# Kernel optimization log

Measured on AMD Instinct MI355X. Metric: run time of the kernel, lower is better.

The kernel has to match this reference:

```python
import jax, jax.numpy as jnp
import numpy as np

N_NODES = 50000
N_EDGES = 600000
DIM = 128
K = 3
N_LAYERS = 3
LEAKY_SLOPE = 0.01  # nn.LeakyReLU default
RE_NORM = 1.0       # 2/lambda_max with lambda_max=2 (standard ChebNet approximation)


def setup_inputs() -> dict:
    key = jax.random.key(0)
    ks = jax.random.split(key, 8)
    weights = jax.random.normal(ks[0], (N_NODES,), dtype=jnp.float32)
    src = jax.random.randint(ks[1], (N_EDGES,), 0, N_NODES)
    dst = jax.random.randint(ks[2], (N_EDGES,), 0, N_NODES)
    lin_in_w = jax.random.normal(ks[3], (1, DIM), dtype=jnp.float32) * 0.5
    lin_in_b = jnp.zeros((DIM,), dtype=jnp.float32)
    cheb_ws = jax.random.normal(ks[4], (N_LAYERS, K * DIM, DIM), dtype=jnp.float32) * 0.05
    cheb_bs = jnp.zeros((N_LAYERS, DIM), dtype=jnp.float32)
    pred_w = jax.random.normal(ks[5], (DIM, 1), dtype=jnp.float32) * 0.05
    pred_b = jnp.zeros((1,), dtype=jnp.float32)
    return {"weights": weights, "src": src, "dst": dst,
            "lin_in_w": lin_in_w, "lin_in_b": lin_in_b,
            "cheb_ws": cheb_ws, "cheb_bs": cheb_bs,
            "pred_w": pred_w, "pred_b": pred_b}


def _cheb_conv(x, W, b, src, dst, d_invsqrt, n):
    # DGL ChebConv with lambda_max=2 -> re_norm=1: scaled Laplacian L_hat = -D^-1/2 A D^-1/2
    def spmm(f):  # unnormalized Laplacian-style aggregation: D^-1/2 A D^-1/2 f
        h = f * d_invsqrt
        agg = jax.ops.segment_sum(h[src], dst, num_segments=n)
        return agg * d_invsqrt

    X0 = x
    terms = [X0]
    h = spmm(X0)
    X1 = -RE_NORM * h + X0 * (RE_NORM - 1.0)
    terms.append(X1)
    for _ in range(2, K):
        h = spmm(X1)
        Xi = -2.0 * RE_NORM * h + X1 * (2.0 * (RE_NORM - 1.0)) - X0
        terms.append(Xi)
        X0, X1 = X1, Xi
    Xt = jnp.concatenate(terms, axis=1)  # [N, K*DIM]
    return jax.nn.relu(Xt @ W + b)       # DGL ChebConv default activation=F.relu


def reference(weights, src, dst, lin_in_w, lin_in_b, cheb_ws, cheb_bs, pred_w, pred_b):
    n = weights.shape[0]
    # dgl.add_self_loop
    loop = jnp.arange(n, dtype=src.dtype)
    src_f = jnp.concatenate([src, loop])
    dst_f = jnp.concatenate([dst, loop])
    # in-degree normalization D^-1/2 (clamp min 1)
    deg = jax.ops.segment_sum(jnp.ones_like(dst_f, dtype=jnp.float32), dst_f, num_segments=n)
    d_invsqrt = jnp.power(jnp.clip(deg, 1.0), -0.5)[:, None]  # [N,1]

    feat = weights[:, None] @ lin_in_w + lin_in_b             # [N, DIM]
    emb = _cheb_conv(feat, cheb_ws[0], cheb_bs[0], src_f, dst_f, d_invsqrt, n)
    for i in range(1, N_LAYERS):
        emb = jax.nn.leaky_relu(emb, negative_slope=LEAKY_SLOPE)
        emb = _cheb_conv(emb, cheb_ws[i], cheb_bs[i], src_f, dst_f, d_invsqrt, n)
    logits = emb @ pred_w + pred_b                            # do_train=True path
    return logits
```

## Files before the change

### kernel.cpp

```cpp
#include <hip/hip_runtime.h>

typedef unsigned int uint;
typedef unsigned short ushort;

#define NN 50000
#define NE 600000
#define DIM 128
#define KD 384
#define PADK 40

typedef __attribute__((ext_vector_type(8))) short short8;
typedef __attribute__((ext_vector_type(4))) float float4v;

static __device__ __forceinline__ ushort f2b(float f) {
    uint u = __float_as_uint(f);
    return (ushort)((u + 0x7FFFu + ((u >> 16) & 1u)) >> 16);
}
static __device__ __forceinline__ float blo(uint u) { return __uint_as_float(u << 16); }
static __device__ __forceinline__ float bhi(uint u) { return __uint_as_float(u & 0xFFFF0000u); }
static __device__ __forceinline__ float asf(uint u) { return __uint_as_float(u); }

__global__ void k_init(int* __restrict__ cnt, const float* __restrict__ cw,
                       ushort* __restrict__ wt, const float* __restrict__ lw,
                       const float* __restrict__ lb, float* __restrict__ uvout) {
    if (blockIdx.x < 49) {
        int i = blockIdx.x * 256 + threadIdx.x;
        if (i < 12544) ((int4*)cnt)[i] = make_int4(0, 0, 0, 0);
    } else if (blockIdx.x < 625) {
        int i = (blockIdx.x - 49) * 256 + threadIdx.x;
        if (i < 3 * KD * DIM) {
            int l = i / (KD * DIM), rem = i - l * (KD * DIM);
            int k = rem >> 7, n = rem & 127;
            wt[(size_t)l * KD * DIM + (size_t)n * KD + k] = f2b(cw[i]);
        }
    } else {
        int vec = blockIdx.x - 625;
        int t = vec >> 1;
        const float* coef = (vec & 1) ? lb : lw;
        int c = threadIdx.x;
        if (c < 128) {
            float s = 0.f;
#pragma unroll 8
            for (int k = 0; k < 128; ++k)
                s = fmaf(coef[k], cw[(size_t)(t * 128 + k) * 128 + c], s);
            uvout[vec * 128 + c] = s;
        }
    }
}

__global__ void k_hist(const int* __restrict__ dst, int* __restrict__ cnt,
                       int* __restrict__ rank) {
    int e = blockIdx.x * 256 + threadIdx.x;
    if (e < NE) rank[e] = atomicAdd(&cnt[dst[e]], 1);
}

__global__ __launch_bounds__(256) void k_scan1(const int* __restrict__ cnt,
                                               int* __restrict__ incl,
                                               int* __restrict__ bsums,
                                               const float* __restrict__ w,
                                               uint2* __restrict__ nrec) {
    __shared__ int sh[256];
    int i = blockIdx.x * 256 + threadIdx.x;
    int v = (i < NN) ? cnt[i] : 0;
    if (i < NN) {
        uint2 r;
        r.x = __float_as_uint(rsqrtf((float)(v + 1)));
        r.y = __float_as_uint(w[i]);
        nrec[i] = r;
    }
    sh[threadIdx.x] = v;
    __syncthreads();
    for (int d = 1; d < 256; d <<= 1) {
        int t = (threadIdx.x >= d) ? sh[threadIdx.x - d] : 0;
        __syncthreads();
        sh[threadIdx.x] += t;
        __syncthreads();
    }
    incl[i] = sh[threadIdx.x];
    if (threadIdx.x == 255) bsums[blockIdx.x] = sh[255];
}

__global__ __launch_bounds__(256) void k_scan3(const int* __restrict__ cnt,
                                               const int* __restrict__ incl,
                                               const int* __restrict__ bsums,
                                               int* __restrict__ offs) {
    __shared__ int sh[256];
    __shared__ int boff;
    int tid = threadIdx.x;
    int v = (tid < 196) ? bsums[tid] : 0;
    sh[tid] = v;
    __syncthreads();
    for (int d = 1; d < 256; d <<= 1) {
        int t = (tid >= d) ? sh[tid - d] : 0;
        __syncthreads();
        sh[tid] += t;
        __syncthreads();
    }
    if (tid == blockIdx.x) boff = sh[tid] - v;
    __syncthreads();
    int i = blockIdx.x * 256 + tid;
    if (i >= NN) return;
    offs[i] = incl[i] - cnt[i] + boff;
    if (i == NN - 1) offs[NN] = NE;
}

__global__ void k_fill4(const int* __restrict__ src, const int* __restrict__ dst,
                        const int* __restrict__ rank, const int* __restrict__ offs,
                        uint* __restrict__ csrS) {
    int e = blockIdx.x * 256 + threadIdx.x;
    if (e < NE) {
        int p = offs[dst[e]] + rank[e];
        csrS[p] = (uint)src[e];
    }
}

__global__ __launch_bounds__(256) void k_csrfin(
        const int* __restrict__ offs, const uint* __restrict__ csrS,
        const uint2* __restrict__ nrec, uint2* __restrict__ csrE,
        float2* __restrict__ SS) {
    int n = blockIdx.x * 16 + (threadIdx.x >> 4);
    int l = threadIdx.x & 15;
    int j0 = offs[n], j1 = offs[n + 1];
    uint2 nr_n = nrec[n];
    float dn = asf(nr_n.x);
    float sA = 0.f, sB = 0.f;
    for (int j = j0 + l; j < j1; j += 16) {
        uint s = csrS[j];
        uint2 nr = nrec[s];
        float ds = asf(nr.x);
        float wv = ds * dn;
        float hw = ds * asf(nr.y);
        uint2 rec;
        rec.x = s;
        rec.y = __float_as_uint(wv);
        csrE[j] = rec;
        sA += hw;
        sB += wv;
    }
#pragma unroll
    for (int off = 8; off > 0; off >>= 1) {
        sA += __shfl_down(sA, off, 16);
        sB += __shfl_down(sB, off, 16);
    }
    if (l == 0) {
        float id = dn * dn;
        float2 o;
        o.x = dn * sA + id * asf(nr_n.y);
        o.y = sB + id;
        SS[n] = o;
    }
}

__global__ __launch_bounds__(256) void k_spmv2l1(
        const int* __restrict__ offs, const uint2* __restrict__ csrE,
        const float2* __restrict__ SS, const uint2* __restrict__ nrec,
        const float* __restrict__ uv, const float* __restrict__ bias,
        ushort* __restrict__ Pb) {
    __shared__ float suv[768];
    __shared__ float sbias[128];
    int tid = threadIdx.x;
    for (int i = tid; i < 768; i += 256) suv[i] = uv[i];
    if (tid < 128) sbias[tid] = bias[tid];
    __syncthreads();

    int n = blockIdx.x * 16 + (tid >> 4);
    int l = tid & 15;
    int j0 = offs[n], j1 = offs[n + 1];
    float sC = 0.f, sD = 0.f;
    for (int j = j0 + l; j < j1; j += 16) {
        uint2 q = csrE[j];
        float wv = asf(q.y);
        float2 s = SS[q.x];
        sC = fmaf(wv, s.x, sC);
        sD = fmaf(wv, s.y, sD);
    }
#pragma unroll
    for (int off = 8; off > 0; off >>= 1) {
        sC += __shfl_down(sC, off, 16);
        sD += __shfl_down(sD, off, 16);
    }
    sC = __shfl(sC, 0, 16);
    sD = __shfl(sD, 0, 16);

    uint2 nr = nrec[n];
    float dn = asf(nr.x), id = dn * dn;
    float2 s = SS[n];
    float ssw = sC + id * s.x;
    float ss1 = sD + id * s.y;
    float a0 = asf(nr.y);
    float a1 = -s.x, b1 = -s.y;
    float a2 = 2.f * ssw - a0, b2 = 2.f * ss1 - 1.f;

    const float2* uv2 = (const float2*)suv;
    uint r[4];
#pragma unroll
    for (int q = 0; q < 4; ++q) {
        int p = 4 * l + q;
        float2 u0 = uv2[p],       v0 = uv2[64 + p];
        float2 u1 = uv2[128 + p], v1 = uv2[192 + p];
        float2 u2 = uv2[256 + p], v2 = uv2[320 + p];
        float2 bb = ((const float2*)sbias)[p];
        float o0 = bb.x + a0 * u0.x + v0.x + a1 * u1.x + b1 * v1.x + a2 * u2.x + b2 * v2.x;
        float o1 = bb.y + a0 * u0.y + v0.y + a1 * u1.y + b1 * v1.y + a2 * u2.y + b2 * v2.y;
        r[q] = (uint)f2b(fmaxf(o0, 0.f)) | ((uint)f2b(fmaxf(o1, 0.f)) << 16);
    }
    uint4 w4; w4.x = r[0]; w4.y = r[1]; w4.z = r[2]; w4.w = r[3];
    ((uint4*)(Pb + (size_t)n * DIM))[l] = w4;
}

__global__ __launch_bounds__(256) void k_gather1(
        const ushort* __restrict__ Xb, const int* __restrict__ offs,
        const uint2* __restrict__ csrE, const uint2* __restrict__ nrec,
        ushort* __restrict__ Qb) {
    int n = __builtin_amdgcn_readfirstlane(blockIdx.x * 4 + (threadIdx.x >> 6));
    int lane = threadIdx.x & 63;
    int j0 = offs[n], j1 = offs[n + 1];
    const uint* Xu = (const uint*)Xb;
    uint un = Xu[(size_t)n * 64 + lane];
    float dn = asf(nrec[n].x);
    float a0 = 0.f, a1 = 0.f;
#pragma unroll 8
    for (int j = j0; j < j1; ++j) {
        uint2 e = csrE[j];
        float wv = asf(e.y);
        uint u = Xu[(size_t)e.x * 64 + lane];
        a0 = fmaf(wv, blo(u), a0);
        a1 = fmaf(wv, bhi(u), a1);
    }
    float id = dn * dn;
    uint ow = (uint)f2b(-(a0 + blo(un) * id))
            | ((uint)f2b(-(a1 + bhi(un) * id)) << 16);
    ((uint*)Qb)[(size_t)n * 64 + lane] = ow;
}

__global__ __launch_bounds__(256) void k_gather2(
        const ushort* __restrict__ X1b, const ushort* __restrict__ X0b,
        const int* __restrict__ offs, const uint2* __restrict__ csrE,
        const uint2* __restrict__ nrec, ushort* __restrict__ Rb) {
    int n = __builtin_amdgcn_readfirstlane(blockIdx.x * 4 + (threadIdx.x >> 6));
    int lane = threadIdx.x & 63;
    int j0 = offs[n], j1 = offs[n + 1];
    const uint* Xu = (const uint*)X1b;
    uint u1n = Xu[(size_t)n * 64 + lane];
    uint u0n = ((const uint*)X0b)[(size_t)n * 64 + lane];
    float dn = asf(nrec[n].x);
    float a0 = 0.f, a1 = 0.f;
#pragma unroll 8
    for (int j = j0; j < j1; ++j) {
        uint2 e = csrE[j];
        float wv = asf(e.y);
        uint u = Xu[(size_t)e.x * 64 + lane];
        a0 = fmaf(wv, blo(u), a0);
        a1 = fmaf(wv, bhi(u), a1);
    }
    float id = dn * dn;
    uint ow = (uint)f2b(-2.f * (a0 + blo(u1n) * id) - blo(u0n))
            | ((uint)f2b(-2.f * (a1 + bhi(u1n) * id) - bhi(u0n)) << 16);
    ((uint*)Rb)[(size_t)n * 64 + lane] = ow;
}

__global__ __launch_bounds__(256) void k_gemm(
        const ushort* __restrict__ X0b, const ushort* __restrict__ X1b,
        const ushort* __restrict__ X2b, const ushort* __restrict__ Wt,
        const float* __restrict__ bias, ushort* __restrict__ outb) {
    __shared__ ushort As[128 * PADK];
    __shared__ ushort Bs[128 * PADK];
    int tid = threadIdx.x;
    int nbase = blockIdx.x * 128;
    int wave = tid >> 6, lane = tid & 63;
    int wr = wave >> 1, wc = wave & 1;
    int l15 = lane & 15, quad = lane >> 4;

    float4v acc[4][4];
#pragma unroll
    for (int i = 0; i < 4; ++i)
#pragma unroll
        for (int j = 0; j < 4; ++j) acc[i][j] = (float4v)0.f;

    int srow = tid >> 1, shalf = tid & 1;
    int gm = nbase + srow; if (gm >= NN) gm = NN - 1;

    for (int c = 0; c < 12; ++c) {
        int part = c >> 2;
        int k0 = (c & 3) * 32;
        const ushort* Xp = (part == 0) ? X0b : ((part == 1) ? X1b : X2b);
        const uint4* ga = (const uint4*)(Xp + (size_t)gm * DIM + k0 + shalf * 16);
        uint4 a0 = ga[0], a1 = ga[1];
        const uint4* gb = (const uint4*)(Wt + (size_t)srow * KD + c * 32 + shalf * 16);
        uint4 b0 = gb[0], b1 = gb[1];
        __syncthreads();
        uint4* pa = (uint4*)(As + srow * PADK + shalf * 16);
        pa[0] = a0; pa[1] = a1;
        uint4* pb = (uint4*)(Bs + srow * PADK + shalf * 16);
        pb[0] = b0; pb[1] = b1;
        __syncthreads();
        short8 af[4], bf[4];
#pragma unroll
        for (int i = 0; i < 4; ++i) {
            af[i] = *(const short8*)(As + (wr * 64 + i * 16 + l15) * PADK + quad * 8);
            bf[i] = *(const short8*)(Bs + (wc * 64 + i * 16 + l15) * PADK + quad * 8);
        }
#pragma unroll
        for (int i = 0; i < 4; ++i)
#pragma unroll
            for (int j = 0; j < 4; ++j)
                acc[i][j] = __builtin_amdgcn_mfma_f32_16x16x32_bf16(
                    af[i], bf[j], acc[i][j], 0, 0, 0);
    }

    float bv[4];
#pragma unroll
    for (int j = 0; j < 4; ++j) bv[j] = bias[wc * 64 + j * 16 + l15];
#pragma unroll
    for (int i = 0; i < 4; ++i) {
#pragma unroll
        for (int r = 0; r < 4; ++r) {
            int node = nbase + wr * 64 + i * 16 + quad * 4 + r;
            if (node < NN) {
#pragma unroll
                for (int j = 0; j < 4; ++j) {
                    int col = wc * 64 + j * 16 + l15;
                    outb[(size_t)node * DIM + col] =
                        f2b(fmaxf(acc[i][j][r] + bv[j], 0.f));
                }
            }
        }
    }
}

__global__ __launch_bounds__(256) void k_gemm_pred(
        const ushort* __restrict__ X0b, const ushort* __restrict__ X1b,
        const ushort* __restrict__ X2b, const ushort* __restrict__ Wt,
        const float* __restrict__ bias, const float* __restrict__ pw,
        const float* __restrict__ pb, float* __restrict__ logits) {
    __shared__ ushort As[128 * PADK];
    __shared__ ushort Bs[128 * PADK];
    __shared__ float lsum[128];
    int tid = threadIdx.x;
    int nbase = blockIdx.x * 128;
    int wave = tid >> 6, lane = tid & 63;
    int wr = wave >> 1, wc = wave & 1;
    int l15 = lane & 15, quad = lane >> 4;

    float4v acc[4][4];
#pragma unroll
    for (int i = 0; i < 4; ++i)
#pragma unroll
        for (int j = 0; j < 4; ++j) acc[i][j] = (float4v)0.f;

    int srow = tid >> 1, shalf = tid & 1;
    int gm = nbase + srow; if (gm >= NN) gm = NN - 1;

    for (int c = 0; c < 12; ++c) {
        int part = c >> 2;
        int k0 = (c & 3) * 32;
        const ushort* Xp = (part == 0) ? X0b : ((part == 1) ? X1b : X2b);
        const uint4* ga = (const uint4*)(Xp + (size_t)gm * DIM + k0 + shalf * 16);
        uint4 a0 = ga[0], a1 = ga[1];
        const uint4* gb = (const uint4*)(Wt + (size_t)srow * KD + c * 32 + shalf * 16);
        uint4 b0 = gb[0], b1 = gb[1];
        __syncthreads();
        uint4* pa = (uint4*)(As + srow * PADK + shalf * 16);
        pa[0] = a0; pa[1] = a1;
        uint4* pb2 = (uint4*)(Bs + srow * PADK + shalf * 16);
        pb2[0] = b0; pb2[1] = b1;
        __syncthreads();
        short8 af[4], bf[4];
#pragma unroll
        for (int i = 0; i < 4; ++i) {
            af[i] = *(const short8*)(As + (wr * 64 + i * 16 + l15) * PADK + quad * 8);
            bf[i] = *(const short8*)(Bs + (wc * 64 + i * 16 + l15) * PADK + quad * 8);
        }
#pragma unroll
        for (int i = 0; i < 4; ++i)
#pragma unroll
            for (int j = 0; j < 4; ++j)
                acc[i][j] = __builtin_amdgcn_mfma_f32_16x16x32_bf16(
                    af[i], bf[j], acc[i][j], 0, 0, 0);
    }

    __syncthreads();
    if (tid < 128) lsum[tid] = 0.f;
    __syncthreads();
    float bv[4], pwv[4];
#pragma unroll
    for (int j = 0; j < 4; ++j) {
        int col = wc * 64 + j * 16 + l15;
        bv[j] = bias[col];
        pwv[j] = pw[col];
    }
#pragma unroll
    for (int i = 0; i < 4; ++i) {
#pragma unroll
        for (int r = 0; r < 4; ++r) {
            float local = 0.f;
#pragma unroll
            for (int j = 0; j < 4; ++j)
                local = fmaf(fmaxf(acc[i][j][r] + bv[j], 0.f), pwv[j], local);
            local += __shfl_xor(local, 1, 64);
            local += __shfl_xor(local, 2, 64);
            local += __shfl_xor(local, 4, 64);
            local += __shfl_xor(local, 8, 64);
            if (l15 == 0)
                atomicAdd(&lsum[wr * 64 + i * 16 + quad * 4 + r], local);
        }
    }
    __syncthreads();
    if (tid < 128) {
        int node = nbase + tid;
        if (node < NN) logits[node] = lsum[tid] + pb[0];
    }
}

extern "C" void kernel_launch(void* const* d_in, const int* in_sizes, int n_in,
                              void* d_out, int out_size, void* d_ws, size_t ws_size,
                              hipStream_t stream) {
    int i_weights = 0, i_src = 1, i_dst = 2, i_lw = 3, i_lb = 4,
        i_cw = 5, i_cb = 6, i_pw = 7, i_pb = 8;
    {
        int seen600k = 0, seen128 = 0;
        for (int i = 0; i < n_in; ++i) {
            int s = in_sizes[i];
            if (s == 50000) i_weights = i;
            else if (s == 600000) { if (seen600k == 0) i_src = i; else i_dst = i; ++seen600k; }
            else if (s == 128) { if (seen128 == 0) i_lw = i; else if (seen128 == 1) i_lb = i; else i_pw = i; ++seen128; }
            else if (s == 147456) i_cw = i;
            else if (s == 384) i_cb = i;
            else if (s == 1) i_pb = i;
        }
    }
    const float* weights = (const float*)d_in[i_weights];
    const int*   src     = (const int*)d_in[i_src];
    const int*   dst     = (const int*)d_in[i_dst];
    const float* lin_w   = (const float*)d_in[i_lw];
    const float* lin_b   = (const float*)d_in[i_lb];
    const float* cheb_w  = (const float*)d_in[i_cw];
    const float* cheb_b  = (const float*)d_in[i_cb];
    const float* pred_w  = (const float*)d_in[i_pw];
    const float* pred_b  = (const float*)d_in[i_pb];
    float* out = (float*)d_out;

    uint2*  csrE    = (uint2*)d_ws;
    uint2*  nrec    = csrE + NE;
    float2* SS      = (float2*)(nrec + 50048);
    float*  uv      = (float*)(SS + 50048);
    int*    offs    = (int*)(uv + 768);
    int*    cnt     = offs + 50056;
    int*    incl    = cnt + 50176;
    int*    bsums   = incl + 50176;
    int*    rank    = bsums + 256;
    uint*   csrS    = (uint*)(rank + NE);
    ushort* Pb      = (ushort*)(csrS + NE);
    ushort* Qb      = Pb + (size_t)NN * DIM;
    ushort* Rb      = Qb + (size_t)NN * DIM;
    ushort* Wtb     = Rb + (size_t)NN * DIM;

    k_init<<<631, 256, 0, stream>>>(cnt, cheb_w, Wtb, lin_w, lin_b, uv);
    k_hist<<<2344, 256, 0, stream>>>(dst, cnt, rank);
    k_scan1<<<196, 256, 0, stream>>>(cnt, incl, bsums, weights, nrec);
    k_scan3<<<196, 256, 0, stream>>>(cnt, incl, bsums, offs);
    k_fill4<<<2344, 256, 0, stream>>>(src, dst, rank, offs, csrS);
    k_csrfin<<<3125, 256, 0, stream>>>(offs, csrS, nrec, csrE, SS);

    k_spmv2l1<<<3125, 256, 0, stream>>>(offs, csrE, SS, nrec, uv, cheb_b, Pb);

    k_gather1<<<12500, 256, 0, stream>>>(Pb, offs, csrE, nrec, Qb);
    k_gather2<<<12500, 256, 0, stream>>>(Qb, Pb, offs, csrE, nrec, Rb);
    k_gemm<<<391, 256, 0, stream>>>(Pb, Qb, Rb, Wtb + (size_t)KD * DIM,
                                    cheb_b + DIM, Pb);
    k_gather1<<<12500, 256, 0, stream>>>(Pb, offs, csrE, nrec, Qb);
    k_gather2<<<12500, 256, 0, stream>>>(Qb, Pb, offs, csrE, nrec, Rb);
    k_gemm_pred<<<391, 256, 0, stream>>>(Pb, Qb, Rb, Wtb + (size_t)2 * KD * DIM,
                                         cheb_b + 2 * DIM, pred_w, pred_b, out);
}
```

Before: 297.9 us.

## Fuse second Chebyshev gather into GEMM via shared-memory X2 tile

Removes the separate k_gather2 kernel. Each GEMM block now computes its own 128 rows of the third Chebyshev term into LDS, using 16 lanes per row with uint4 loads, and feeds them to the MFMA loop. This drops the global write and re-read of the X2 buffer and one launch per layer. In exchange the latency-bound sparse gather runs on only 391 blocks, with heavier LDS use per block, so occupancy and memory-level parallelism for the gather phase fall.

```diff
diff --git a/kernel.cpp b/kernel.cpp
--- a/kernel.cpp
+++ b/kernel.cpp
@@ -8,6 +8,7 @@
 #define DIM 128
 #define KD 384
 #define PADK 40
+#define X2P 136
 
 typedef __attribute__((ext_vector_type(8))) short short8;
 typedef __attribute__((ext_vector_type(4))) float float4v;
@@ -233,40 +234,60 @@
     ((uint*)Qb)[(size_t)n * 64 + lane] = ow;
 }
 
-__global__ __launch_bounds__(256) void k_gather2(
-        const ushort* __restrict__ X1b, const ushort* __restrict__ X0b,
+__global__ __launch_bounds__(256) void k_gemmf(
+        const ushort* __restrict__ X0b, const ushort* __restrict__ X1b,
         const int* __restrict__ offs, const uint2* __restrict__ csrE,
-        const uint2* __restrict__ nrec, ushort* __restrict__ Rb) {
-    int n = __builtin_amdgcn_readfirstlane(blockIdx.x * 4 + (threadIdx.x >> 6));
-    int lane = threadIdx.x & 63;
-    int j0 = offs[n], j1 = offs[n + 1];
-    const uint* Xu = (const uint*)X1b;
-    uint u1n = Xu[(size_t)n * 64 + lane];
-    uint u0n = ((const uint*)X0b)[(size_t)n * 64 + lane];
-    float dn = asf(nrec[n].x);
-    float a0 = 0.f, a1 = 0.f;
-#pragma unroll 8
-    for (int j = j0; j < j1; ++j) {
-        uint2 e = csrE[j];
-        float wv = asf(e.y);
-        uint u = Xu[(size_t)e.x * 64 + lane];
-        a0 = fmaf(wv, blo(u), a0);
-        a1 = fmaf(wv, bhi(u), a1);
-    }
-    float id = dn * dn;
-    uint ow = (uint)f2b(-2.f * (a0 + blo(u1n) * id) - blo(u0n))
-            | ((uint)f2b(-2.f * (a1 + bhi(u1n) * id) - bhi(u0n)) << 16);
-    ((uint*)Rb)[(size_t)n * 64 + lane] = ow;
-}
-
-__global__ __launch_bounds__(256) void k_gemm(
-        const ushort* __restrict__ X0b, const ushort* __restrict__ X1b,
-        const ushort* __restrict__ X2b, const ushort* __restrict__ Wt,
+        const uint2* __restrict__ nrec, const ushort* __restrict__ Wt,
         const float* __restrict__ bias, ushort* __restrict__ outb) {
     __shared__ ushort As[128 * PADK];
     __shared__ ushort Bs[128 * PADK];
+    __shared__ ushort X2s[128 * X2P];
     int tid = threadIdx.x;
     int nbase = blockIdx.x * 128;
+
+    {
+        int grp = tid >> 4;
+        int l = tid & 15;
+        const uint4* X1u4 = (const uint4*)X1b;
+        const uint4* X0u4 = (const uint4*)X0b;
+        for (int k = 0; k < 8; ++k) {
+            int row = grp * 8 + k;
+            int n = nbase + row;
+            uint4 w4;
+            if (n < NN) {
+                int j0 = offs[n], j1 = offs[n + 1];
+                float a0 = 0.f, a1 = 0.f, a2 = 0.f, a3 = 0.f;
+                float a4 = 0.f, a5 = 0.f, a6 = 0.f, a7 = 0.f;
+#pragma unroll 4
+                for (int j = j0; j < j1; ++j) {
+                    uint2 e = csrE[j];
+                    float wv = asf(e.y);
+                    uint4 u = X1u4[(size_t)e.x * 16 + l];
+                    a0 = fmaf(wv, blo(u.x), a0); a1 = fmaf(wv, bhi(u.x), a1);
+                    a2 = fmaf(wv, blo(u.y), a2); a3 = fmaf(wv, bhi(u.y), a3);
+                    a4 = fmaf(wv, blo(u.z), a4); a5 = fmaf(wv, bhi(u.z), a5);
+                    a6 = fmaf(wv, blo(u.w), a6); a7 = fmaf(wv, bhi(u.w), a7);
+                }
+                float dn = asf(nrec[n].x);
+                float id = dn * dn;
+                uint4 u1 = X1u4[(size_t)n * 16 + l];
+                uint4 u0 = X0u4[(size_t)n * 16 + l];
+                w4.x = (uint)f2b(-2.f * (a0 + blo(u1.x) * id) - blo(u0.x))
+                     | ((uint)f2b(-2.f * (a1 + bhi(u1.x) * id) - bhi(u0.x)) << 16);
+                w4.y = (uint)f2b(-2.f * (a2 + blo(u1.y) * id) - blo(u0.y))
+                     | ((uint)f2b(-2.f * (a3 + bhi(u1.y) * id) - bhi(u0.y)) << 16);
+                w4.z = (uint)f2b(-2.f * (a4 + blo(u1.z) * id) - blo(u0.z))
+                     | ((uint)f2b(-2.f * (a5 + bhi(u1.z) * id) - bhi(u0.z)) << 16);
+                w4.w = (uint)f2b(-2.f * (a6 + blo(u1.w) * id) - blo(u0.w))
+                     | ((uint)f2b(-2.f * (a7 + bhi(u1.w) * id) - bhi(u0.w)) << 16);
+            } else {
+                w4.x = 0; w4.y = 0; w4.z = 0; w4.w = 0;
+            }
+            *(uint4*)(X2s + (size_t)row * X2P + l * 8) = w4;
+        }
+    }
+    __syncthreads();
+
     int wave = tid >> 6, lane = tid & 63;
     int wr = wave >> 1, wc = wave & 1;
     int l15 = lane & 15, quad = lane >> 4;
@@ -283,21 +304,30 @@
     for (int c = 0; c < 12; ++c) {
         int part = c >> 2;
         int k0 = (c & 3) * 32;
-        const ushort* Xp = (part == 0) ? X0b : ((part == 1) ? X1b : X2b);
-        const uint4* ga = (const uint4*)(Xp + (size_t)gm * DIM + k0 + shalf * 16);
-        uint4 a0 = ga[0], a1 = ga[1];
+        uint4 a0, a1;
+        if (part < 2) {
+            const ushort* Xp = (part == 0) ? X0b : X1b;
+            const uint4* ga = (const uint4*)(Xp + (size_t)gm * DIM + k0 + shalf * 16);
+            a0 = ga[0]; a1 = ga[1];
+        }
         const uint4* gb = (const uint4*)(Wt + (size_t)srow * KD + c * 32 + shalf * 16);
         uint4 b0 = gb[0], b1 = gb[1];
         __syncthreads();
-        uint4* pa = (uint4*)(As + srow * PADK + shalf * 16);
-        pa[0] = a0; pa[1] = a1;
+        if (part < 2) {
+            uint4* pa = (uint4*)(As + srow * PADK + shalf * 16);
+            pa[0] = a0; pa[1] = a1;
+        }
         uint4* pb = (uint4*)(Bs + srow * PADK + shalf * 16);
         pb[0] = b0; pb[1] = b1;
         __syncthreads();
         short8 af[4], bf[4];
 #pragma unroll
         for (int i = 0; i < 4; ++i) {
-            af[i] = *(const short8*)(As + (wr * 64 + i * 16 + l15) * PADK + quad * 8);
+            if (part < 2)
+                af[i] = *(const short8*)(As + (wr * 64 + i * 16 + l15) * PADK + quad * 8);
+            else
+                af[i] = *(const short8*)(X2s + (size_t)(wr * 64 + i * 16 + l15) * X2P
+                                         + k0 + quad * 8);
             bf[i] = *(const short8*)(Bs + (wc * 64 + i * 16 + l15) * PADK + quad * 8);
         }
 #pragma unroll
@@ -328,16 +358,62 @@
     }
 }
 
-__global__ __launch_bounds__(256) void k_gemm_pred(
+__global__ __launch_bounds__(256) void k_gemmf_pred(
         const ushort* __restrict__ X0b, const ushort* __restrict__ X1b,
-        const ushort* __restrict__ X2b, const ushort* __restrict__ Wt,
+        const int* __restrict__ offs, const uint2* __restrict__ csrE,
+        const uint2* __restrict__ nrec, const ushort* __restrict__ Wt,
         const float* __restrict__ bias, const float* __restrict__ pw,
         const float* __restrict__ pb, float* __restrict__ logits) {
     __shared__ ushort As[128 * PADK];
     __shared__ ushort Bs[128 * PADK];
+    __shared__ ushort X2s[128 * X2P];
     __shared__ float lsum[128];
     int tid = threadIdx.x;
     int nbase = blockIdx.x * 128;
+
+    {
+        int grp = tid >> 4;
+        int l = tid & 15;
+        const uint4* X1u4 = (const uint4*)X1b;
+        const uint4* X0u4 = (const uint4*)X0b;
+        for (int k = 0; k < 8; ++k) {
+            int row = grp * 8 + k;
+            int n = nbase + row;
+            uint4 w4;
+            if (n < NN) {
+                int j0 = offs[n], j1 = offs[n + 1];
+                float a0 = 0.f, a1 = 0.f, a2 = 0.f, a3 = 0.f;
+                float a4 = 0.f, a5 = 0.f, a6 = 0.f, a7 = 0.f;
+#pragma unroll 4
+                for (int j = j0; j < j1; ++j) {
+                    uint2 e = csrE[j];
+                    float wv = asf(e.y);
+                    uint4 u = X1u4[(size_t)e.x * 16 + l];
+                    a0 = fmaf(wv, blo(u.x), a0); a1 = fmaf(wv, bhi(u.x), a1);
+                    a2 = fmaf(wv, blo(u.y), a2); a3 = fmaf(wv, bhi(u.y), a3);
+                    a4 = fmaf(wv, blo(u.z), a4); a5 = fmaf(wv, bhi(u.z), a5);
+                    a6 = fmaf(wv, blo(u.w), a6); a7 = fmaf(wv, bhi(u.w), a7);
+                }
+                float dn = asf(nrec[n].x);
+                float id = dn * dn;
+                uint4 u1 = X1u4[(size_t)n * 16 + l];
+                uint4 u0 = X0u4[(size_t)n * 16 + l];
+                w4.x = (uint)f2b(-2.f * (a0 + blo(u1.x) * id) - blo(u0.x))
+                     | ((uint)f2b(-2.f * (a1 + bhi(u1.x) * id) - bhi(u0.x)) << 16);
+                w4.y = (uint)f2b(-2.f * (a2 + blo(u1.y) * id) - blo(u0.y))
+                     | ((uint)f2b(-2.f * (a3 + bhi(u1.y) * id) - bhi(u0.y)) << 16);
+                w4.z = (uint)f2b(-2.f * (a4 + blo(u1.z) * id) - blo(u0.z))
+                     | ((uint)f2b(-2.f * (a5 + bhi(u1.z) * id) - bhi(u0.z)) << 16);
+                w4.w = (uint)f2b(-2.f * (a6 + blo(u1.w) * id) - blo(u0.w))
+                     | ((uint)f2b(-2.f * (a7 + bhi(u1.w) * id) - bhi(u0.w)) << 16);
+            } else {
+                w4.x = 0; w4.y = 0; w4.z = 0; w4.w = 0;
+            }
+            *(uint4*)(X2s + (size_t)row * X2P + l * 8) = w4;
+        }
+    }
+    __syncthreads();
+
     int wave = tid >> 6, lane = tid & 63;
     int wr = wave >> 1, wc = wave & 1;
     int l15 = lane & 15, quad = lane >> 4;
@@ -354,21 +430,30 @@
     for (int c = 0; c < 12; ++c) {
         int part = c >> 2;
         int k0 = (c & 3) * 32;
-        const ushort* Xp = (part == 0) ? X0b : ((part == 1) ? X1b : X2b);
-        const uint4* ga = (const uint4*)(Xp + (size_t)gm * DIM + k0 + shalf * 16);
-        uint4 a0 = ga[0], a1 = ga[1];
+        uint4 a0, a1;
+        if (part < 2) {
+            const ushort* Xp = (part == 0) ? X0b : X1b;
+            const uint4* ga = (const uint4*)(Xp + (size_t)gm * DIM + k0 + shalf * 16);
+            a0 = ga[0]; a1 = ga[1];
+        }
         const uint4* gb = (const uint4*)(Wt + (size_t)srow * KD + c * 32 + shalf * 16);
         uint4 b0 = gb[0], b1 = gb[1];
         __syncthreads();
-        uint4* pa = (uint4*)(As + srow * PADK + shalf * 16);
-        pa[0] = a0; pa[1] = a1;
+        if (part < 2) {
+            uint4* pa = (uint4*)(As + srow * PADK + shalf * 16);
+            pa[0] = a0; pa[1] = a1;
+        }
         uint4* pb2 = (uint4*)(Bs + srow * PADK + shalf * 16);
         pb2[0] = b0; pb2[1] = b1;
         __syncthreads();
         short8 af[4], bf[4];
 #pragma unroll
         for (int i = 0; i < 4; ++i) {
-            af[i] = *(const short8*)(As + (wr * 64 + i * 16 + l15) * PADK + quad * 8);
+            if (part < 2)
+                af[i] = *(const short8*)(As + (wr * 64 + i * 16 + l15) * PADK + quad * 8);
+            else
+                af[i] = *(const short8*)(X2s + (size_t)(wr * 64 + i * 16 + l15) * X2P
+                                         + k0 + quad * 8);
             bf[i] = *(const short8*)(Bs + (wc * 64 + i * 16 + l15) * PADK + quad * 8);
         }
 #pragma unroll
@@ -452,8 +537,7 @@
     uint*   csrS    = (uint*)(rank + NE);
     ushort* Pb      = (ushort*)(csrS + NE);
     ushort* Qb      = Pb + (size_t)NN * DIM;
-    ushort* Rb      = Qb + (size_t)NN * DIM;
-    ushort* Wtb     = Rb + (size_t)NN * DIM;
+    ushort* Wtb     = Qb + (size_t)NN * DIM;
 
     k_init<<<631, 256, 0, stream>>>(cnt, cheb_w, Wtb, lin_w, lin_b, uv);
     k_hist<<<2344, 256, 0, stream>>>(dst, cnt, rank);
@@ -465,11 +549,10 @@
     k_spmv2l1<<<3125, 256, 0, stream>>>(offs, csrE, SS, nrec, uv, cheb_b, Pb);
 
     k_gather1<<<12500, 256, 0, stream>>>(Pb, offs, csrE, nrec, Qb);
-    k_gather2<<<12500, 256, 0, stream>>>(Qb, Pb, offs, csrE, nrec, Rb);
-    k_gemm<<<391, 256, 0, stream>>>(Pb, Qb, Rb, Wtb + (size_t)KD * DIM,
-                                    cheb_b + DIM, Pb);
+    k_gemmf<<<391, 256, 0, stream>>>(Pb, Qb, offs, csrE, nrec,
+                                     Wtb + (size_t)KD * DIM, cheb_b + DIM, Pb);
     k_gather1<<<12500, 256, 0, stream>>>(Pb, offs, csrE, nrec, Qb);
-    k_gather2<<<12500, 256, 0, stream>>>(Qb, Pb, offs, csrE, nrec, Rb);
-    k_gemm_pred<<<391, 256, 0, stream>>>(Pb, Qb, Rb, Wtb + (size_t)2 * KD * DIM,
-                                         cheb_b + 2 * DIM, pred_w, pred_b, out);
-}
+    k_gemmf_pred<<<391, 256, 0, stream>>>(Pb, Qb, offs, csrE, nrec,
+                                          Wtb + (size_t)2 * KD * DIM,
+                                          cheb_b + 2 * DIM, pred_w, pred_b, out);
+}
```

New measurement: 321.9 us. 1.08x slower.
